# Optimization experiments

Measured on AMD Instinct MI355X. Metric: run time of the kernel, lower is better.

## Reference

```python
import jax, jax.numpy as jnp
import numpy as np

N, E = 50000, 800000
IN, H, OUT = 128, 128, 64
N_MID = 4  # middle GIN layers (num_layers=6 -> 1 first + 4 mid + 1 last)


def setup_inputs() -> dict:
    key = jax.random.key(0)
    ks = jax.random.split(key, 8)
    def w(k, shape, fan_in):
        return (jax.random.normal(k, shape, jnp.float32) / np.sqrt(fan_in)).astype(jnp.float32)
    x = jax.random.normal(ks[0], (N, IN), jnp.float32)
    edge_index = jax.random.randint(ks[1], (2, E), 0, N, dtype=jnp.int64)
    return {
        "x": x,
        "edge_index": edge_index,
        "w0a": w(ks[2], (IN, H), IN), "b0a": jnp.zeros((H,), jnp.float32),
        "w0b": w(ks[3], (H, H), H),   "b0b": jnp.zeros((H,), jnp.float32),
        "wma": w(ks[4], (N_MID, H, H), H), "bma": jnp.zeros((N_MID, H), jnp.float32),
        "wmb": w(ks[5], (N_MID, H, H), H), "bmb": jnp.zeros((N_MID, H), jnp.float32),
        "wl": w(ks[6], (H, OUT), H), "bl": jnp.zeros((OUT,), jnp.float32),
    }


def reference(x, edge_index, w0a, b0a, w0b, b0b, wma, bma, wmb, bmb, wl, bl):
    n = x.shape[0]
    src, dst = edge_index[0], edge_index[1]

    def gin_agg(h):
        # GIN with eps=0: (1+eps)*h_i + sum_{j->i} h_j
        return h + jax.ops.segment_sum(h[src], dst, num_segments=n)

    # layer 0: Lin(IN,H)-ReLU-Lin(H,H), then inter-layer ReLU
    h = gin_agg(x)
    h = jax.nn.relu(jax.nn.relu(h @ w0a + b0a) @ w0b + b0b)

    # middle layers 1..4 (scan over stacked params)
    def body(h, p):
        wa, ba, wb, bb = p
        g = gin_agg(h)
        g = jax.nn.relu(g @ wa + ba) @ wb + bb
        return jax.nn.relu(g), None

    h, _ = jax.lax.scan(body, h, (wma, bma, wmb, bmb))

    # last layer: single Lin(H,OUT), then sigmoid
    h = gin_agg(h) @ wl + bl
    return jax.nn.sigmoid(h)
```

## Files before the change

kernel.cpp:

```cpp
#include <hip/hip_runtime.h>
#include <hip/hip_bf16.h>

#define HDIM 128

typedef __attribute__((ext_vector_type(8))) short bf16x8;
typedef __attribute__((ext_vector_type(4))) float f32x4;

__device__ __forceinline__ unsigned short bf16_rne(float x) {
    unsigned int u = __float_as_uint(x);
    unsigned int r = u + 0x7FFFu + ((u >> 16) & 1u);
    return (unsigned short)(r >> 16);
}


__global__ __launch_bounds__(256) void hist_kernel(const int* __restrict__ ei, int E,
                                                   int* __restrict__ deg) {
    int e = blockIdx.x * 256 + threadIdx.x;
    if (e < E) atomicAdd(&deg[ei[E + e]], 1);
}

__global__ __launch_bounds__(256) void scan1_kernel(const int* __restrict__ deg,
                                                    int* __restrict__ rowp,
                                                    int* __restrict__ bsum, int N) {
    __shared__ int s[256];
    int t = threadIdx.x;
    int i = blockIdx.x * 256 + t;
    int v = (i < N) ? deg[i] : 0;
    s[t] = v; __syncthreads();
    for (int off = 1; off < 256; off <<= 1) {
        int x = (t >= off) ? s[t - off] : 0;
        __syncthreads();
        s[t] += x;
        __syncthreads();
    }
    if (i < N) rowp[i] = s[t] - v;
    if (t == 255) bsum[blockIdx.x] = s[255];
}

__global__ __launch_bounds__(256) void scan2_kernel(int* __restrict__ bsum, int NB) {
    __shared__ int s[256];
    int t = threadIdx.x;
    int v = (t < NB) ? bsum[t] : 0;
    s[t] = v; __syncthreads();
    for (int off = 1; off < 256; off <<= 1) {
        int x = (t >= off) ? s[t - off] : 0;
        __syncthreads();
        s[t] += x;
        __syncthreads();
    }
    if (t < NB) bsum[t] = s[t] - v;
}

__global__ __launch_bounds__(256) void scan3_kernel(int* __restrict__ rowp,
                                                    const int* __restrict__ bsum,
                                                    int* __restrict__ cur, int N, int E) {
    int i = blockIdx.x * 256 + threadIdx.x;
    if (i < N) {
        int r = rowp[i] + bsum[blockIdx.x];
        rowp[i] = r;
        cur[i] = r;
    }
    if (i == 0) rowp[N] = E;
}

template <typename IT>
__global__ __launch_bounds__(256) void scatter_kernel(const int* __restrict__ ei, int E,
                                                      int* __restrict__ cur,
                                                      IT* __restrict__ srcs) {
    int e = blockIdx.x * 256 + threadIdx.x;
    if (e < E) {
        int d = ei[E + e];
        int p = atomicAdd(&cur[d], 1);
        srcs[p] = (IT)ei[e];
    }
}


__global__ __launch_bounds__(256) void pack_w_kernel(const float* __restrict__ w0a,
                                                     const float* __restrict__ w0b,
                                                     const float* __restrict__ wma,
                                                     const float* __restrict__ wmb,
                                                     short* __restrict__ wpack) {
    int idx = blockIdx.x * 256 + threadIdx.x;
    if (idx >= 10 * 16384) return;
    int mat = idx >> 14;
    int rem = idx & 16383;
    int i = rem & 7;
    int lane = (rem >> 3) & 63;
    int kc = (rem >> 9) & 3;
    int ct = rem >> 11;
    const float* W = (mat == 0) ? w0a
                   : (mat == 1) ? w0b
                   : (mat < 6)  ? (wma + (size_t)(mat - 2) * 16384)
                                : (wmb + (size_t)(mat - 6) * 16384);
    int k = kc * 32 + (lane >> 4) * 8 + i;
    int col = ct * 16 + (lane & 15);
    float x = W[k * 128 + col];
    unsigned short hb = bf16_rne(x);
    float hf = __uint_as_float(((unsigned int)hb) << 16);
    unsigned short lb = bf16_rne(x - hf);
    wpack[(size_t)mat * 32768 + rem] = (short)hb;
    wpack[(size_t)mat * 32768 + 16384 + rem] = (short)lb;
}


template <typename IT>
__global__ __launch_bounds__(256) void agg_kernel(const float* __restrict__ h,
                                                  const int* __restrict__ rowp,
                                                  const IT* __restrict__ srcs,
                                                  float* __restrict__ out, int N) {
    const int tid  = threadIdx.x;
    const int lane = tid & 63;
    const int half = lane >> 5;
    const int l    = lane & 31;
    const int node = blockIdx.x * 8 + ((tid >> 6) << 1) + half;
    const bool nv  = node < N;
    const int nc   = nv ? node : 0;

    const float4* h4 = (const float4*)h;
    int beg = rowp[nc];
    int end = nv ? rowp[nc + 1] : beg;
    int em1 = max(end - 1, 0);

    const float4 z = {0.f, 0.f, 0.f, 0.f};
    float4 a0 = nv ? h4[(size_t)nc * 32 + l] : z;
    float4 a1 = z, a2 = z, a3 = z, a4 = z, a5 = z, a6 = z, a7 = z;

    for (int q = beg; q < end; q += 8) {
        int c0 = min(q + 0, em1);
        int c1 = min(q + 1, em1);
        int c2 = min(q + 2, em1);
        int c3 = min(q + 3, em1);
        int c4 = min(q + 4, em1);
        int c5 = min(q + 5, em1);
        int c6 = min(q + 6, em1);
        int c7 = min(q + 7, em1);
        int s0 = (int)srcs[c0];
        int s1 = (int)srcs[c1];
        int s2 = (int)srcs[c2];
        int s3 = (int)srcs[c3];
        int s4 = (int)srcs[c4];
        int s5 = (int)srcs[c5];
        int s6 = (int)srcs[c6];
        int s7 = (int)srcs[c7];
        float4 v0 = h4[(size_t)s0 * 32 + l];
        float4 v1 = h4[(size_t)s1 * 32 + l];
        float4 v2 = h4[(size_t)s2 * 32 + l];
        float4 v3 = h4[(size_t)s3 * 32 + l];
        float4 v4 = h4[(size_t)s4 * 32 + l];
        float4 v5 = h4[(size_t)s5 * 32 + l];
        float4 v6 = h4[(size_t)s6 * 32 + l];
        float4 v7 = h4[(size_t)s7 * 32 + l];
        float m0 = (q + 0 < end) ? 1.f : 0.f;
        float m1 = (q + 1 < end) ? 1.f : 0.f;
        float m2 = (q + 2 < end) ? 1.f : 0.f;
        float m3 = (q + 3 < end) ? 1.f : 0.f;
        float m4 = (q + 4 < end) ? 1.f : 0.f;
        float m5 = (q + 5 < end) ? 1.f : 0.f;
        float m6 = (q + 6 < end) ? 1.f : 0.f;
        float m7 = (q + 7 < end) ? 1.f : 0.f;
        a0.x = fmaf(v0.x, m0, a0.x); a0.y = fmaf(v0.y, m0, a0.y);
        a0.z = fmaf(v0.z, m0, a0.z); a0.w = fmaf(v0.w, m0, a0.w);
        a1.x = fmaf(v1.x, m1, a1.x); a1.y = fmaf(v1.y, m1, a1.y);
        a1.z = fmaf(v1.z, m1, a1.z); a1.w = fmaf(v1.w, m1, a1.w);
        a2.x = fmaf(v2.x, m2, a2.x); a2.y = fmaf(v2.y, m2, a2.y);
        a2.z = fmaf(v2.z, m2, a2.z); a2.w = fmaf(v2.w, m2, a2.w);
        a3.x = fmaf(v3.x, m3, a3.x); a3.y = fmaf(v3.y, m3, a3.y);
        a3.z = fmaf(v3.z, m3, a3.z); a3.w = fmaf(v3.w, m3, a3.w);
        a4.x = fmaf(v4.x, m4, a4.x); a4.y = fmaf(v4.y, m4, a4.y);
        a4.z = fmaf(v4.z, m4, a4.z); a4.w = fmaf(v4.w, m4, a4.w);
        a5.x = fmaf(v5.x, m5, a5.x); a5.y = fmaf(v5.y, m5, a5.y);
        a5.z = fmaf(v5.z, m5, a5.z); a5.w = fmaf(v5.w, m5, a5.w);
        a6.x = fmaf(v6.x, m6, a6.x); a6.y = fmaf(v6.y, m6, a6.y);
        a6.z = fmaf(v6.z, m6, a6.z); a6.w = fmaf(v6.w, m6, a6.w);
        a7.x = fmaf(v7.x, m7, a7.x); a7.y = fmaf(v7.y, m7, a7.y);
        a7.z = fmaf(v7.z, m7, a7.z); a7.w = fmaf(v7.w, m7, a7.w);
    }

    a0.x = ((a0.x + a1.x) + (a2.x + a3.x)) + ((a4.x + a5.x) + (a6.x + a7.x));
    a0.y = ((a0.y + a1.y) + (a2.y + a3.y)) + ((a4.y + a5.y) + (a6.y + a7.y));
    a0.z = ((a0.z + a1.z) + (a2.z + a3.z)) + ((a4.z + a5.z) + (a6.z + a7.z));
    a0.w = ((a0.w + a1.w) + (a2.w + a3.w)) + ((a4.w + a5.w) + (a6.w + a7.w));
    if (nv) ((float4*)out)[(size_t)node * 32 + l] = a0;
}


template <typename IT>
__global__ __launch_bounds__(256) void agg_out_kernel(const float* __restrict__ t,
                                                      const int* __restrict__ rowp,
                                                      const IT* __restrict__ srcs,
                                                      const float* __restrict__ bias,
                                                      float* __restrict__ out, int N) {
    int lane = threadIdx.x & 63;
    int node = blockIdx.x * 4 + (threadIdx.x >> 6);
    if (node >= N) return;
    int beg = rowp[node], end = rowp[node + 1];
    float a0 = t[node * 64 + lane];
    float a1 = 0.f, a2 = 0.f, a3 = 0.f, a4 = 0.f, a5 = 0.f, a6 = 0.f, a7 = 0.f;
    int p = beg;
    for (; p + 8 <= end; p += 8) {
        int s0 = (int)srcs[p + 0];
        int s1 = (int)srcs[p + 1];
        int s2 = (int)srcs[p + 2];
        int s3 = (int)srcs[p + 3];
        int s4 = (int)srcs[p + 4];
        int s5 = (int)srcs[p + 5];
        int s6 = (int)srcs[p + 6];
        int s7 = (int)srcs[p + 7];
        a0 += t[s0 * 64 + lane];
        a1 += t[s1 * 64 + lane];
        a2 += t[s2 * 64 + lane];
        a3 += t[s3 * 64 + lane];
        a4 += t[s4 * 64 + lane];
        a5 += t[s5 * 64 + lane];
        a6 += t[s6 * 64 + lane];
        a7 += t[s7 * 64 + lane];
    }
    for (; p < end; ++p) a0 += t[(int)srcs[p] * 64 + lane];
    float z = a0 + ((a1 + a2) + (a3 + a4)) + ((a5 + a6) + a7) + bias[lane];
    out[node * 64 + lane] = 1.f / (1.f + __expf(-z));
}


__device__ __forceinline__ void cvt8(const float4 p, const float4 q,
                                     bf16x8& hi, bf16x8& lo) {
    unsigned short hb; float hf;
#define CVT1(IDX, V) \
    hb = bf16_rne(V); hf = __uint_as_float(((unsigned int)hb) << 16); \
    hi[IDX] = (short)hb; lo[IDX] = (short)bf16_rne((V) - hf);
    CVT1(0, p.x) CVT1(1, p.y) CVT1(2, p.z) CVT1(3, p.w)
    CVT1(4, q.x) CVT1(5, q.y) CVT1(6, q.z) CVT1(7, q.w)
#undef CVT1
}

template <bool WRITE_GLOBAL>
__device__ __forceinline__ void gemm_phase_mfma(float* __restrict__ myrows,
                                                const short* __restrict__ wp,
                                                const float* __restrict__ bias,
                                                int arow, int agrp,
                                                int l, float* __restrict__ gout,
                                                int row_base, int N) {
    f32x4 acc[8];
#pragma unroll
    for (int ct = 0; ct < 8; ++ct) acc[ct] = (f32x4){0.f, 0.f, 0.f, 0.f};

    const short* wlo = wp + 16384;
#pragma unroll
    for (int kc = 0; kc < 4; ++kc) {
        const float* ap = &myrows[arow * 132 + kc * 32 + agrp * 8];
        float4 p = *(const float4*)ap;
        float4 q = *(const float4*)(ap + 4);
        bf16x8 ahi, alo;
        cvt8(p, q, ahi, alo);
#pragma unroll
        for (int ct = 0; ct < 8; ++ct) {
            const int off = ((ct * 4 + kc) << 9) + (l << 3);
            bf16x8 bhi = *(const bf16x8*)(wp + off);
            bf16x8 blo = *(const bf16x8*)(wlo + off);
            acc[ct] = __builtin_amdgcn_mfma_f32_16x16x32_bf16(ahi, bhi, acc[ct], 0, 0, 0);
            acc[ct] = __builtin_amdgcn_mfma_f32_16x16x32_bf16(alo, bhi, acc[ct], 0, 0, 0);
            acc[ct] = __builtin_amdgcn_mfma_f32_16x16x32_bf16(ahi, blo, acc[ct], 0, 0, 0);
            acc[ct] = __builtin_amdgcn_mfma_f32_16x16x32_bf16(alo, blo, acc[ct], 0, 0, 0);
        }
    }

#pragma unroll
    for (int ct = 0; ct < 8; ++ct) {
        float bv = bias[ct * 16 + arow];
#pragma unroll
        for (int r = 0; r < 4; ++r) {
            float v = fmaxf(acc[ct][r] + bv, 0.f);
            if (WRITE_GLOBAL) {
                int row = row_base + agrp * 4 + r;
                if (row < N) gout[(size_t)row * 128 + ct * 16 + arow] = v;
            } else {
                myrows[(agrp * 4 + r) * 132 + ct * 16 + arow] = v;
            }
        }
    }
}

__global__ __launch_bounds__(256, 4) void mlp2_mfma_kernel(
    const float* __restrict__ in,
    const short* __restrict__ wpa, const float* __restrict__ ba,
    const short* __restrict__ wpb, const float* __restrict__ bb,
    float* __restrict__ out, int N) {
    __shared__ float sh[64 * 132];
    const int tid = threadIdx.x;
    const int wave = tid >> 6;
    const int l = tid & 63;
    const int arow = l & 15;
    const int agrp = l >> 4;
    const int row0 = blockIdx.x * 64;

    const float4* in4 = (const float4*)in;
#pragma unroll
    for (int it = 0; it < 8; ++it) {
        int i = tid + it * 256;
        int r = i >> 5, c = i & 31;
        int row = row0 + r;
        float4 z = {0.f, 0.f, 0.f, 0.f};
        float4 v = (row < N) ? in4[(size_t)row * 32 + c] : z;
        *(float4*)&sh[r * 132 + c * 4] = v;
    }
    __syncthreads();

    float* myrows = &sh[wave * 16 * 132];
    gemm_phase_mfma<false>(myrows, wpa, ba, arow, agrp, l, nullptr, 0, N);
    __syncthreads();
    gemm_phase_mfma<true>(myrows, wpb, bb, arow, agrp, l, out, row0 + wave * 16, N);
}


__global__ __launch_bounds__(256, 6) void gemm64_kernel(const float* __restrict__ in,
                                                        const float* __restrict__ W,
                                                        float* __restrict__ out, int N) {
    constexpr int TX = 16, RPT = 2;
    __shared__ float4 sh[32 * 32];

    int tid = threadIdx.x;
    int tx = tid % TX;
    int ty = tid / TX;
    int row0 = blockIdx.x * 32;

    const float4* in4 = (const float4*)in;
    for (int i = tid; i < 32 * 32; i += 256) {
        int r = i >> 5, c = i & 31;
        int row = row0 + r;
        float4 z = {0.f, 0.f, 0.f, 0.f};
        sh[i] = (row < N) ? in4[(size_t)row * 32 + c] : z;
    }
    __syncthreads();

    const float4* W4 = (const float4*)W;
    float acc[RPT][4];
#pragma unroll
    for (int r = 0; r < RPT; ++r)
#pragma unroll
        for (int c = 0; c < 4; ++c) acc[r][c] = 0.f;

#pragma unroll 4
    for (int kk = 0; kk < 128; kk += 4) {
        float4 w0 = W4[(kk + 0) * TX + tx];
        float4 w1 = W4[(kk + 1) * TX + tx];
        float4 w2 = W4[(kk + 2) * TX + tx];
        float4 w3 = W4[(kk + 3) * TX + tx];
#pragma unroll
        for (int r = 0; r < RPT; ++r) {
            float4 hv = sh[(ty * RPT + r) * 32 + (kk >> 2)];
            acc[r][0] += hv.x * w0.x + hv.y * w1.x + hv.z * w2.x + hv.w * w3.x;
            acc[r][1] += hv.x * w0.y + hv.y * w1.y + hv.z * w2.y + hv.w * w3.y;
            acc[r][2] += hv.x * w0.z + hv.y * w1.z + hv.z * w2.z + hv.w * w3.z;
            acc[r][3] += hv.x * w0.w + hv.y * w1.w + hv.z * w2.w + hv.w * w3.w;
        }
    }

#pragma unroll
    for (int r = 0; r < RPT; ++r) {
        int row = row0 + ty * RPT + r;
        if (row < N) {
            float4 v = {acc[r][0], acc[r][1], acc[r][2], acc[r][3]};
            ((float4*)out)[(size_t)row * TX + tx] = v;
        }
    }
}


template <typename IT>
static void run_graph(const float* x, const int* ei, int N, int E,
                      const float* w0a, const float* b0a, const float* w0b, const float* b0b,
                      const float* wma, const float* bma, const float* wmb, const float* bmb,
                      const float* wl, const float* bl,
                      float* A, float* B, int* deg, int* rowp, int* cur, int* bsum,
                      IT* srcs, short* wpack, float* out, hipStream_t stream) {
    const int NB = (N + 255) / 256;
    dim3 blk(256);

    pack_w_kernel<<<(10 * 16384 + 255) / 256, blk, 0, stream>>>(w0a, w0b, wma, wmb, wpack);

    hipMemsetAsync(deg, 0, (size_t)N * sizeof(int), stream);
    hist_kernel<<<(E + 255) / 256, blk, 0, stream>>>(ei, E, deg);
    scan1_kernel<<<NB, blk, 0, stream>>>(deg, rowp, bsum, N);
    scan2_kernel<<<1, blk, 0, stream>>>(bsum, NB);
    scan3_kernel<<<NB, blk, 0, stream>>>(rowp, bsum, cur, N, E);
    scatter_kernel<IT><<<(E + 255) / 256, blk, 0, stream>>>(ei, E, cur, srcs);

    const int agg_grid  = (N + 7) / 8;
    const int aggo_grid = (N + 3) / 4;
    const int m64_grid  = (N + 63) / 64;
    const int g32_grid  = (N + 31) / 32;

    agg_kernel<IT><<<agg_grid, blk, 0, stream>>>(x, rowp, srcs, A, N);
    mlp2_mfma_kernel<<<m64_grid, blk, 0, stream>>>(A, wpack + 0, b0a,
                                                   wpack + 32768, b0b, B, N);

    float* h = B;
    float* o = A;
    for (int l = 0; l < 4; ++l) {
        const short* wpa = wpack + (size_t)(2 + l) * 32768;
        const short* wpb = wpack + (size_t)(6 + l) * 32768;
        const float* ba = bma + (size_t)l * HDIM;
        const float* bb = bmb + (size_t)l * HDIM;
        agg_kernel<IT><<<agg_grid, blk, 0, stream>>>(h, rowp, srcs, o, N);
        mlp2_mfma_kernel<<<m64_grid, blk, 0, stream>>>(o, wpa, ba, wpb, bb, h, N);
    }

    gemm64_kernel<<<g32_grid, blk, 0, stream>>>(h, wl, o, N);
    agg_out_kernel<IT><<<aggo_grid, blk, 0, stream>>>(o, rowp, srcs, bl, out, N);
}

extern "C" void kernel_launch(void* const* d_in, const int* in_sizes, int n_in,
                              void* d_out, int out_size, void* d_ws, size_t ws_size,
                              hipStream_t stream) {
    const float* x   = (const float*)d_in[0];
    const int*   ei  = (const int*)d_in[1];
    const float* w0a = (const float*)d_in[2];
    const float* b0a = (const float*)d_in[3];
    const float* w0b = (const float*)d_in[4];
    const float* b0b = (const float*)d_in[5];
    const float* wma = (const float*)d_in[6];
    const float* bma = (const float*)d_in[7];
    const float* wmb = (const float*)d_in[8];
    const float* bmb = (const float*)d_in[9];
    const float* wl  = (const float*)d_in[10];
    const float* bl  = (const float*)d_in[11];

    const int N = in_sizes[0] / HDIM;
    const int E = in_sizes[1] / 2;

    float* A = (float*)d_ws;
    float* B = A + (size_t)N * HDIM;
    int* deg  = (int*)(B + (size_t)N * HDIM);
    int* rowp = deg + N;
    int* cur  = rowp + N + 1;
    int* bsum = cur + N;
    int* srcs = bsum + 256;
    short* wpack = (short*)(srcs + E);

    if (N <= 65535) {
        run_graph<unsigned short>(x, ei, N, E, w0a, b0a, w0b, b0b, wma, bma, wmb, bmb,
                                  wl, bl, A, B, deg, rowp, cur, bsum,
                                  (unsigned short*)srcs, wpack, (float*)d_out, stream);
    } else {
        run_graph<int>(x, ei, N, E, w0a, b0a, w0b, b0b, wma, bma, wmb, bmb,
                       wl, bl, A, B, deg, rowp, cur, bsum,
                       srcs, wpack, (float*)d_out, stream);
    }
}
```

Before: 594.4 us.

## Split aggregation into column slices so each block gathers a 64-byte feature slice

Replaces the per-node aggregation, where 32 lanes gather a full 512-byte row, with a sliced kernel. Each of 8 blocks per 64-node chunk handles one 16-float column slice, and 4 lanes per node read 64 bytes per neighbor. Consecutive blocks work on the same node chunk, so the intent is better L2 locality: at any moment the working set is a narrow column slice of h. The cost is that rowp and srcs are read 8 times, and each gather is a smaller 64-byte access, which may use memory transactions less efficiently.

```diff
diff --git a/kernel.cpp b/kernel.cpp
--- a/kernel.cpp
+++ b/kernel.cpp
@@ -105,25 +105,26 @@
 
 
 template <typename IT>
-__global__ __launch_bounds__(256) void agg_kernel(const float* __restrict__ h,
-                                                  const int* __restrict__ rowp,
-                                                  const IT* __restrict__ srcs,
-                                                  float* __restrict__ out, int N) {
-    const int tid  = threadIdx.x;
-    const int lane = tid & 63;
-    const int half = lane >> 5;
-    const int l    = lane & 31;
-    const int node = blockIdx.x * 8 + ((tid >> 6) << 1) + half;
-    const bool nv  = node < N;
-    const int nc   = nv ? node : 0;
+__global__ __launch_bounds__(256) void agg_slice_kernel(const float* __restrict__ h,
+                                                        const int* __restrict__ rowp,
+                                                        const IT* __restrict__ srcs,
+                                                        float* __restrict__ out, int N) {
+    const int tid = threadIdx.x;
+    const int g = blockIdx.x & 7;
+    const int chunk = blockIdx.x >> 3;
+    const int grp = tid >> 2;
+    const int l = tid & 3;
+    const int node = chunk * 64 + grp;
+    if (node >= N) return;
 
     const float4* h4 = (const float4*)h;
-    int beg = rowp[nc];
-    int end = nv ? rowp[nc + 1] : beg;
+    const int cbase = g * 4 + l;
+
+    int beg = rowp[node], end = rowp[node + 1];
     int em1 = max(end - 1, 0);
 
     const float4 z = {0.f, 0.f, 0.f, 0.f};
-    float4 a0 = nv ? h4[(size_t)nc * 32 + l] : z;
+    float4 a0 = h4[(size_t)node * 32 + cbase];
     float4 a1 = z, a2 = z, a3 = z, a4 = z, a5 = z, a6 = z, a7 = z;
 
     for (int q = beg; q < end; q += 8) {
@@ -143,14 +144,14 @@
         int s5 = (int)srcs[c5];
         int s6 = (int)srcs[c6];
         int s7 = (int)srcs[c7];
-        float4 v0 = h4[(size_t)s0 * 32 + l];
-        float4 v1 = h4[(size_t)s1 * 32 + l];
-        float4 v2 = h4[(size_t)s2 * 32 + l];
-        float4 v3 = h4[(size_t)s3 * 32 + l];
-        float4 v4 = h4[(size_t)s4 * 32 + l];
-        float4 v5 = h4[(size_t)s5 * 32 + l];
-        float4 v6 = h4[(size_t)s6 * 32 + l];
-        float4 v7 = h4[(size_t)s7 * 32 + l];
+        float4 v0 = h4[(size_t)s0 * 32 + cbase];
+        float4 v1 = h4[(size_t)s1 * 32 + cbase];
+        float4 v2 = h4[(size_t)s2 * 32 + cbase];
+        float4 v3 = h4[(size_t)s3 * 32 + cbase];
+        float4 v4 = h4[(size_t)s4 * 32 + cbase];
+        float4 v5 = h4[(size_t)s5 * 32 + cbase];
+        float4 v6 = h4[(size_t)s6 * 32 + cbase];
+        float4 v7 = h4[(size_t)s7 * 32 + cbase];
         float m0 = (q + 0 < end) ? 1.f : 0.f;
         float m1 = (q + 1 < end) ? 1.f : 0.f;
         float m2 = (q + 2 < end) ? 1.f : 0.f;
@@ -181,7 +182,7 @@
     a0.y = ((a0.y + a1.y) + (a2.y + a3.y)) + ((a4.y + a5.y) + (a6.y + a7.y));
     a0.z = ((a0.z + a1.z) + (a2.z + a3.z)) + ((a4.z + a5.z) + (a6.z + a7.z));
     a0.w = ((a0.w + a1.w) + (a2.w + a3.w)) + ((a4.w + a5.w) + (a6.w + a7.w));
-    if (nv) ((float4*)out)[(size_t)node * 32 + l] = a0;
+    ((float4*)out)[(size_t)node * 32 + cbase] = a0;
 }
 
 
@@ -385,12 +386,12 @@
     scan3_kernel<<<NB, blk, 0, stream>>>(rowp, bsum, cur, N, E);
     scatter_kernel<IT><<<(E + 255) / 256, blk, 0, stream>>>(ei, E, cur, srcs);
 
-    const int agg_grid  = (N + 7) / 8;
-    const int aggo_grid = (N + 3) / 4;
-    const int m64_grid  = (N + 63) / 64;
-    const int g32_grid  = (N + 31) / 32;
-
-    agg_kernel<IT><<<agg_grid, blk, 0, stream>>>(x, rowp, srcs, A, N);
+    const int slice_grid = 8 * ((N + 63) / 64);
+    const int aggo_grid  = (N + 3) / 4;
+    const int m64_grid   = (N + 63) / 64;
+    const int g32_grid   = (N + 31) / 32;
+
+    agg_slice_kernel<IT><<<slice_grid, blk, 0, stream>>>(x, rowp, srcs, A, N);
     mlp2_mfma_kernel<<<m64_grid, blk, 0, stream>>>(A, wpack + 0, b0a,
                                                    wpack + 32768, b0b, B, N);
 
@@ -401,7 +402,7 @@
         const short* wpb = wpack + (size_t)(6 + l) * 32768;
         const float* ba = bma + (size_t)l * HDIM;
         const float* bb = bmb + (size_t)l * HDIM;
-        agg_kernel<IT><<<agg_grid, blk, 0, stream>>>(h, rowp, srcs, o, N);
+        agg_slice_kernel<IT><<<slice_grid, blk, 0, stream>>>(h, rowp, srcs, o, N);
         mlp2_mfma_kernel<<<m64_grid, blk, 0, stream>>>(o, wpa, ba, wpb, bb, h, N);
     }
 
```

Result: slower. 666.5 us (+12.1%).
